# Kernel tuning notes

Hardware: AMD Instinct MI355X
Metric: run time of the kernel (lower is better)

## Reference

```python
import jax, jax.numpy as jnp
import numpy as np
from jax import lax


def _b_mask(out_c, in_c, kh, kw):
    # MaskedConv2d mask_type='B' for a 1xK kernel: zero strictly right-of-center taps
    m = np.ones((out_c, in_c, kh, kw), dtype=np.float32)
    m[:, :, kh // 2:, kw // 2 + 1:] = 0
    m[:, :, kh // 2 + 1:, :] = 0
    return jnp.asarray(m)


def _conv(x, w, b):
    # NCHW 'same' conv, stride 1
    y = lax.conv_general_dilated(x, w, (1, 1), 'SAME',
                                 dimension_numbers=('NCHW', 'OIHW', 'NCHW'))
    return y + b[None, :, None, None]


def setup_inputs() -> dict:
    key = jax.random.key(0)
    ks = jax.random.split(key, 7)
    B, C_in, H, W = 32, 3, 64, 64
    HC = 128
    return {
        'x': jax.random.normal(ks[0], (B, C_in, H, W), jnp.float32),
        'W_is': jax.random.normal(ks[1], (4 * HC, C_in, 1, 3), jnp.float32) * 0.1,
        'b_is': jax.random.normal(ks[2], (4 * HC,), jnp.float32) * 0.1,
        'W_ss': jax.random.normal(ks[3], (4 * HC, HC, 1, 3), jnp.float32) * 0.1,
        'b_ss': jax.random.normal(ks[4], (4 * HC,), jnp.float32) * 0.1,
        'h0': jax.random.normal(ks[5], (1, HC, 1, W), jnp.float32) * 0.05,
        'c0': jax.random.normal(ks[6], (1, HC, 1, W), jnp.float32) * 0.05,
    }


def reference(x, W_is, b_is, W_ss, b_ss, h0, c0):
    B, _, H, W = x.shape
    HC = h0.shape[1]
    W_is_m = W_is * _b_mask(*W_is.shape)
    W_ss_m = W_ss * _b_mask(*W_ss.shape)

    # input-to-state projection for all rows at once: [B, 4*HC, H, W]
    x_proj = _conv(x, W_is_m, b_is)
    x_rows = jnp.moveaxis(x_proj, 2, 0)[:, :, :, None, :]  # [H, B, 4HC, 1, W]

    h_init = jnp.broadcast_to(h0, (B, HC, 1, W))
    c_init = jnp.broadcast_to(c0, (B, HC, 1, W))

    def step(carry, row_x):
        h_prev, c_prev = carry
        gates = jax.nn.sigmoid(row_x + _conv(h_prev, W_ss_m, b_ss))
        o, f, i, g = jnp.split(gates, 4, axis=1)
        c = f * c_prev + i * g
        h = o * jnp.tanh(c)
        return (h, c), h

    _, hs = lax.scan(step, (h_init, c_init), x_rows)  # hs: [H, B, HC, 1, W]
    hidden = jnp.moveaxis(hs[:, :, :, 0, :], 0, 2)  # [B, HC, H, W]
    return hidden
```

## Files before the change

### kernel.cpp

```cpp
#include <hip/hip_runtime.h>
#include <hip/hip_bf16.h>

typedef unsigned short u16;
typedef unsigned int u32;
typedef unsigned long long u64;
typedef short bf16x8 __attribute__((ext_vector_type(8)));
typedef float f32x4  __attribute__((ext_vector_type(4)));


__device__ __forceinline__ u16 f2b(float f) {
    return __builtin_bit_cast(u16, __float2bfloat16(f));
}
__device__ __forceinline__ float sigm(float x) {
    return __builtin_amdgcn_rcpf(1.0f + __expf(-x));
}

#define LINE(kt, lane) (((kt) * 64 + (lane)) * 16)
#define BUFBYTES (8 * 64 * 16)
#define SPIN_CAP (1 << 16)

__global__ __launch_bounds__(512, 2) void rowlstm_mfma13(
    const float* __restrict__ x,   const float* __restrict__ Wis,
    const float* __restrict__ bis, const float* __restrict__ Wss,
    const float* __restrict__ bss, const float* __restrict__ h0,
    const float* __restrict__ c0,  float* __restrict__ out,
    char* halo)
{
    __shared__ __align__(16) char lds_buf[2 * BUFBYTES];
    __shared__ __align__(16) char lds_xpk[64 * 16 * 16];
    __shared__ u16  lds_x[3 * 64 * 17];
    __shared__ float lds_bias[512];

    const int tid  = threadIdx.x;
    const int s    = blockIdx.x;
    const int b    = blockIdx.y;
    const int wid  = tid >> 6;
    const int lane = tid & 63;
    const int q    = lane >> 4;
    const int n    = lane & 15;
    const int wbase = s * 16;

    char* hs_my = halo + ((size_t)(b * 4 + s) * 64) * 256;
    char* hs_up = halo + ((size_t)(b * 4 + (s > 0 ? s - 1 : 0)) * 64) * 256;

    for (int i = tid; i < 1024; i += 512)
        *(uint4*)(lds_buf + i * 16) = make_uint4(0, 0, 0, 0);
    __syncthreads();

    lds_bias[tid] = bis[tid] + bss[tid];

    for (int i = tid; i < 3264; i += 512) {
        int cch = i / 1088, rem = i % 1088;
        int r = rem / 17, wl1 = rem % 17;
        int gw = wbase + wl1 - 1;
        lds_x[i] = (gw < 0) ? (u16)0
                 : f2b(x[(((size_t)b * 3 + cch) * 64 + r) * 64 + gw]);
    }

    bf16x8 afr[4][9];
    {
        #pragma unroll
        for (int g = 0; g < 4; ++g) {
            int oc = g * 128 + wid * 16 + n;
            #pragma unroll
            for (int kt = 0; kt < 8; ++kt) {
                bf16x8 a;
                #pragma unroll
                for (int jj = 0; jj < 4; ++jj) {
                    int ic = kt * 16 + q * 4 + jj;
                    float2 wp = *(const float2*)&Wss[(size_t)(oc * 128 + ic) * 3];
                    a[jj]     = (short)f2b(wp.y);
                    a[4 + jj] = (short)f2b(wp.x);
                }
                afr[g][kt] = a;
            }
            bf16x8 ax = {0, 0, 0, 0, 0, 0, 0, 0};
            if (q == 0) {
                #pragma unroll
                for (int cch = 0; cch < 3; ++cch) {
                    float2 wp = *(const float2*)&Wis[(size_t)(oc * 3 + cch) * 3];
                    ax[cch]     = (short)f2b(wp.y);
                    ax[4 + cch] = (short)f2b(wp.x);
                }
            }
            afr[g][8] = ax;
        }
    }

    float cst[4];
    {
        u16 hw[4];
        #pragma unroll
        for (int reg = 0; reg < 4; ++reg) {
            int hc = wid * 16 + q * 4 + reg;
            int wg = wbase + n;
            cst[reg] = c0[hc * 64 + wg];
            hw[reg] = f2b(h0[hc * 64 + wg]);
        }
        u64 d01 = (u64)((u32)hw[0] | ((u32)hw[1] << 16))
                | ((u64)((u32)hw[2] | ((u32)hw[3] << 16)) << 32);
        *(u64*)(lds_buf + LINE(wid, lane)) = d01;
        int wl = n + 1;
        if (wl < 16)
            *(u64*)(lds_buf + LINE(wid, q * 16 + wl) + 8) = d01;
    }
    if (s > 0 && tid < 32) {
        int ic0 = tid * 4;
        u64 v = (u64)((u32)f2b(h0[(ic0 + 0) * 64 + wbase - 1]) | ((u32)f2b(h0[(ic0 + 1) * 64 + wbase - 1]) << 16))
              | ((u64)((u32)f2b(h0[(ic0 + 2) * 64 + wbase - 1]) | ((u32)f2b(h0[(ic0 + 3) * 64 + wbase - 1]) << 16)) << 32);
        *(u64*)(lds_buf + LINE(tid >> 2, (tid & 3) * 16) + 8) = v;
    }

    __syncthreads();

    #pragma unroll
    for (int t = 0; t < 2; ++t) {
        int slot = tid + t * 512;
        int r = slot >> 4, nn = slot & 15;
        u32 d0 = (u32)lds_x[0 * 1088 + r * 17 + nn + 1] | ((u32)lds_x[1 * 1088 + r * 17 + nn + 1] << 16);
        u32 d1 = (u32)lds_x[2 * 1088 + r * 17 + nn + 1];
        u32 d2 = (u32)lds_x[0 * 1088 + r * 17 + nn]     | ((u32)lds_x[1 * 1088 + r * 17 + nn] << 16);
        u32 d3 = (u32)lds_x[2 * 1088 + r * 17 + nn];
        *(uint4*)(lds_xpk + slot * 16) = make_uint4(d0, d1, d2, d3);
    }
    __syncthreads();

    f32x4 bias_r[4];
    #pragma unroll
    for (int g = 0; g < 4; ++g) {
        int oc = g * 128 + wid * 16 + q * 4;
        bias_r[g][0] = lds_bias[oc + 0];
        bias_r[g][1] = lds_bias[oc + 1];
        bias_r[g][2] = lds_bias[oc + 2];
        bias_r[g][3] = lds_bias[oc + 3];
    }

    u64 hv = 0, hn = 0;
    const bool is_cons = (s > 0) && (tid < 32);
    if (is_cons)
        hv = __hip_atomic_load((const u64*)(hs_up + (size_t)tid * 8),
                               __ATOMIC_RELAXED, __HIP_MEMORY_SCOPE_AGENT);

    for (int r = 0; r < 64; ++r) {
        char* rbuf = lds_buf + (r & 1) * BUFBYTES;
        char* wbuf = lds_buf + ((r & 1) ^ 1) * BUFBYTES;

        if (is_cons && r < 62)
            hn = __hip_atomic_load((const u64*)(hs_up + (size_t)(r + 1) * 256 + tid * 8),
                                   __ATOMIC_RELAXED, __HIP_MEMORY_SCOPE_AGENT);

        bf16x8 bv[9];
        #pragma unroll
        for (int kt = 0; kt < 8; ++kt)
            bv[kt] = *(const bf16x8*)(rbuf + LINE(kt, lane));
        bv[8] = *(const bf16x8*)(lds_xpk + r * 256 + n * 16);

        f32x4 acc[4];
        acc[0] = bias_r[0]; acc[1] = bias_r[1];
        acc[2] = bias_r[2]; acc[3] = bias_r[3];
        #pragma unroll
        for (int kt = 0; kt < 9; ++kt) {
            acc[0] = __builtin_amdgcn_mfma_f32_16x16x32_bf16(afr[0][kt], bv[kt], acc[0], 0, 0, 0);
            acc[1] = __builtin_amdgcn_mfma_f32_16x16x32_bf16(afr[1][kt], bv[kt], acc[1], 0, 0, 0);
            acc[2] = __builtin_amdgcn_mfma_f32_16x16x32_bf16(afr[2][kt], bv[kt], acc[2], 0, 0, 0);
            acc[3] = __builtin_amdgcn_mfma_f32_16x16x32_bf16(afr[3][kt], bv[kt], acc[3], 0, 0, 0);
        }

        float hval[4];
        #pragma unroll
        for (int reg = 0; reg < 4; ++reg) {
            float eo = __expf(-acc[0][reg]);
            float ef = __expf(-acc[1][reg]);
            float ei = __expf(-acc[2][reg]);
            float eg = __expf(-acc[3][reg]);
            float f_ = __builtin_amdgcn_rcpf(1.0f + ef);
            float t  = 1.0f + ei;
            float ig = __builtin_amdgcn_rcpf(__builtin_fmaf(eg, t, t));
            float cn = f_ * cst[reg] + ig;
            cst[reg] = cn;
            float o_ = __builtin_amdgcn_rcpf(1.0f + eo);
            float e2 = __expf(2.0f * cn);
            float th = 1.0f - 2.0f * __builtin_amdgcn_rcpf(e2 + 1.0f);
            hval[reg] = o_ * th;
        }

        u32 plo, phi;
        asm("v_cvt_pk_bf16_f32 %0, %1, %2" : "=v"(plo) : "v"(hval[0]), "v"(hval[1]));
        asm("v_cvt_pk_bf16_f32 %0, %1, %2" : "=v"(phi) : "v"(hval[2]), "v"(hval[3]));
        u64 d01 = (u64)plo | ((u64)phi << 32);

        *(u64*)(wbuf + LINE(wid, lane)) = d01;
        int wl = n + 1;
        if (wl < 16) {
            *(u64*)(wbuf + LINE(wid, q * 16 + wl) + 8) = d01;
        } else if (s < 3 && r < 63) {
            __hip_atomic_store((u64*)(hs_my + (size_t)r * 256 + (wid * 4 + q) * 8),
                               ~d01, __ATOMIC_RELAXED, __HIP_MEMORY_SCOPE_AGENT);
        }

        #pragma unroll
        for (int reg = 0; reg < 4; ++reg) {
            int hc = wid * 16 + q * 4 + reg;
            out[(((size_t)(b * 128 + hc)) * 64 + r) * 64 + wbase + n] = hval[reg];
        }

        if (is_cons && r < 63) {
            if (hv == 0) {
                int guard = 0;
                do {
                    __builtin_amdgcn_s_sleep(1);
                    hv = __hip_atomic_load((const u64*)(hs_up + (size_t)r * 256 + tid * 8),
                                           __ATOMIC_RELAXED, __HIP_MEMORY_SCOPE_AGENT);
                } while (hv == 0 && ++guard < SPIN_CAP);
            }
            *(u64*)(wbuf + LINE(tid >> 2, (tid & 3) * 16) + 8) = ~hv;
            hv = hn;
        }

        __builtin_amdgcn_sched_barrier(0);
        asm volatile("s_waitcnt lgkmcnt(0)\n\ts_barrier" ::: "memory");
        __builtin_amdgcn_sched_barrier(0);
    }
}

extern "C" void kernel_launch(void* const* d_in, const int* in_sizes, int n_in,
                              void* d_out, int out_size, void* d_ws, size_t ws_size,
                              hipStream_t stream)
{
    const float* x   = (const float*)d_in[0];
    const float* Wis = (const float*)d_in[1];
    const float* bis = (const float*)d_in[2];
    const float* Wss = (const float*)d_in[3];
    const float* bss = (const float*)d_in[4];
    const float* h0  = (const float*)d_in[5];
    const float* c0  = (const float*)d_in[6];
    float* out = (float*)d_out;

    hipMemsetAsync(d_ws, 0, (size_t)32 * 4 * 64 * 256, stream);
    rowlstm_mfma13<<<dim3(4, 32), 512, 0, stream>>>(
        x, Wis, bis, Wss, bss, h0, c0, out, (char*)d_ws);
}
```

Measured before the change: 203.2 us.

## Split gate computation across 16 waves with LDS flag handoff for i*g

Doubles the workgroup to 1024 threads. Back waves compute the input and cell gates (i, g) and pass i*g to front waves through LDS, signalled by a per-wave flag. Front waves compute o and f and carry out the cell/hidden update, the halo exchange and the output stores. This halves the MFMA chain and weight registers per wave to cut per-row latency on the serial recurrence, at the cost of intra-workgroup spin-waiting and an extra LDS round trip.

```diff
diff --git a/kernel.cpp b/kernel.cpp
--- a/kernel.cpp
+++ b/kernel.cpp
@@ -11,15 +11,12 @@
 __device__ __forceinline__ u16 f2b(float f) {
     return __builtin_bit_cast(u16, __float2bfloat16(f));
 }
-__device__ __forceinline__ float sigm(float x) {
-    return __builtin_amdgcn_rcpf(1.0f + __expf(-x));
-}
 
 #define LINE(kt, lane) (((kt) * 64 + (lane)) * 16)
 #define BUFBYTES (8 * 64 * 16)
 #define SPIN_CAP (1 << 16)
 
-__global__ __launch_bounds__(512, 2) void rowlstm_mfma13(
+__global__ __launch_bounds__(1024, 1) void rowlstm_mfma14(
     const float* __restrict__ x,   const float* __restrict__ Wis,
     const float* __restrict__ bis, const float* __restrict__ Wss,
     const float* __restrict__ bss, const float* __restrict__ h0,
@@ -28,13 +25,17 @@
 {
     __shared__ __align__(16) char lds_buf[2 * BUFBYTES];
     __shared__ __align__(16) char lds_xpk[64 * 16 * 16];
+    __shared__ __align__(16) char lds_igb[8 * 64 * 16];
     __shared__ u16  lds_x[3 * 64 * 17];
     __shared__ float lds_bias[512];
+    __shared__ u32  igf[8];
 
     const int tid  = threadIdx.x;
     const int s    = blockIdx.x;
     const int b    = blockIdx.y;
     const int wid  = tid >> 6;
+    const int p    = wid & 7;
+    const bool front = (wid < 8);
     const int lane = tid & 63;
     const int q    = lane >> 4;
     const int n    = lane & 15;
@@ -43,13 +44,14 @@
     char* hs_my = halo + ((size_t)(b * 4 + s) * 64) * 256;
     char* hs_up = halo + ((size_t)(b * 4 + (s > 0 ? s - 1 : 0)) * 64) * 256;
 
-    for (int i = tid; i < 1024; i += 512)
-        *(uint4*)(lds_buf + i * 16) = make_uint4(0, 0, 0, 0);
+    if (tid < 1024)
+        *(uint4*)(lds_buf + tid * 16) = make_uint4(0, 0, 0, 0);
+    if (tid < 8) igf[tid] = 0;
     __syncthreads();
 
-    lds_bias[tid] = bis[tid] + bss[tid];
-
-    for (int i = tid; i < 3264; i += 512) {
+    if (tid < 512) lds_bias[tid] = bis[tid] + bss[tid];
+
+    for (int i = tid; i < 3264; i += 1024) {
         int cch = i / 1088, rem = i % 1088;
         int r = rem / 17, wl1 = rem % 17;
         int gw = wbase + wl1 - 1;
@@ -57,11 +59,12 @@
                  : f2b(x[(((size_t)b * 3 + cch) * 64 + r) * 64 + gw]);
     }
 
-    bf16x8 afr[4][9];
+    const int gbase = front ? 0 : 2;
+    bf16x8 afr[2][9];
     {
         #pragma unroll
-        for (int g = 0; g < 4; ++g) {
-            int oc = g * 128 + wid * 16 + n;
+        for (int gg = 0; gg < 2; ++gg) {
+            int oc = (gbase + gg) * 128 + p * 16 + n;
             #pragma unroll
             for (int kt = 0; kt < 8; ++kt) {
                 bf16x8 a;
@@ -72,7 +75,7 @@
                     a[jj]     = (short)f2b(wp.y);
                     a[4 + jj] = (short)f2b(wp.x);
                 }
-                afr[g][kt] = a;
+                afr[gg][kt] = a;
             }
             bf16x8 ax = {0, 0, 0, 0, 0, 0, 0, 0};
             if (q == 0) {
@@ -83,26 +86,26 @@
                     ax[4 + cch] = (short)f2b(wp.x);
                 }
             }
-            afr[g][8] = ax;
-        }
-    }
-
-    float cst[4];
-    {
+            afr[gg][8] = ax;
+        }
+    }
+
+    float cst[4] = {0, 0, 0, 0};
+    if (front) {
         u16 hw[4];
         #pragma unroll
         for (int reg = 0; reg < 4; ++reg) {
-            int hc = wid * 16 + q * 4 + reg;
+            int hc = p * 16 + q * 4 + reg;
             int wg = wbase + n;
             cst[reg] = c0[hc * 64 + wg];
             hw[reg] = f2b(h0[hc * 64 + wg]);
         }
         u64 d01 = (u64)((u32)hw[0] | ((u32)hw[1] << 16))
                 | ((u64)((u32)hw[2] | ((u32)hw[3] << 16)) << 32);
-        *(u64*)(lds_buf + LINE(wid, lane)) = d01;
+        *(u64*)(lds_buf + LINE(p, lane)) = d01;
         int wl = n + 1;
         if (wl < 16)
-            *(u64*)(lds_buf + LINE(wid, q * 16 + wl) + 8) = d01;
+            *(u64*)(lds_buf + LINE(p, q * 16 + wl) + 8) = d01;
     }
     if (s > 0 && tid < 32) {
         int ic0 = tid * 4;
@@ -113,9 +116,8 @@
 
     __syncthreads();
 
-    #pragma unroll
-    for (int t = 0; t < 2; ++t) {
-        int slot = tid + t * 512;
+    {
+        int slot = tid;
         int r = slot >> 4, nn = slot & 15;
         u32 d0 = (u32)lds_x[0 * 1088 + r * 17 + nn + 1] | ((u32)lds_x[1 * 1088 + r * 17 + nn + 1] << 16);
         u32 d1 = (u32)lds_x[2 * 1088 + r * 17 + nn + 1];
@@ -125,14 +127,14 @@
     }
     __syncthreads();
 
-    f32x4 bias_r[4];
+    f32x4 bias_r[2];
     #pragma unroll
-    for (int g = 0; g < 4; ++g) {
-        int oc = g * 128 + wid * 16 + q * 4;
-        bias_r[g][0] = lds_bias[oc + 0];
-        bias_r[g][1] = lds_bias[oc + 1];
-        bias_r[g][2] = lds_bias[oc + 2];
-        bias_r[g][3] = lds_bias[oc + 3];
+    for (int gg = 0; gg < 2; ++gg) {
+        int oc = (gbase + gg) * 128 + p * 16 + q * 4;
+        bias_r[gg][0] = lds_bias[oc + 0];
+        bias_r[gg][1] = lds_bias[oc + 1];
+        bias_r[gg][2] = lds_bias[oc + 2];
+        bias_r[gg][3] = lds_bias[oc + 3];
     }
 
     u64 hv = 0, hn = 0;
@@ -155,66 +157,91 @@
             bv[kt] = *(const bf16x8*)(rbuf + LINE(kt, lane));
         bv[8] = *(const bf16x8*)(lds_xpk + r * 256 + n * 16);
 
-        f32x4 acc[4];
+        f32x4 acc[2];
         acc[0] = bias_r[0]; acc[1] = bias_r[1];
-        acc[2] = bias_r[2]; acc[3] = bias_r[3];
         #pragma unroll
         for (int kt = 0; kt < 9; ++kt) {
             acc[0] = __builtin_amdgcn_mfma_f32_16x16x32_bf16(afr[0][kt], bv[kt], acc[0], 0, 0, 0);
             acc[1] = __builtin_amdgcn_mfma_f32_16x16x32_bf16(afr[1][kt], bv[kt], acc[1], 0, 0, 0);
-            acc[2] = __builtin_amdgcn_mfma_f32_16x16x32_bf16(afr[2][kt], bv[kt], acc[2], 0, 0, 0);
-            acc[3] = __builtin_amdgcn_mfma_f32_16x16x32_bf16(afr[3][kt], bv[kt], acc[3], 0, 0, 0);
-        }
-
-        float hval[4];
-        #pragma unroll
-        for (int reg = 0; reg < 4; ++reg) {
-            float eo = __expf(-acc[0][reg]);
-            float ef = __expf(-acc[1][reg]);
-            float ei = __expf(-acc[2][reg]);
-            float eg = __expf(-acc[3][reg]);
-            float f_ = __builtin_amdgcn_rcpf(1.0f + ef);
-            float t  = 1.0f + ei;
-            float ig = __builtin_amdgcn_rcpf(__builtin_fmaf(eg, t, t));
-            float cn = f_ * cst[reg] + ig;
-            cst[reg] = cn;
-            float o_ = __builtin_amdgcn_rcpf(1.0f + eo);
-            float e2 = __expf(2.0f * cn);
-            float th = 1.0f - 2.0f * __builtin_amdgcn_rcpf(e2 + 1.0f);
-            hval[reg] = o_ * th;
-        }
-
-        u32 plo, phi;
-        asm("v_cvt_pk_bf16_f32 %0, %1, %2" : "=v"(plo) : "v"(hval[0]), "v"(hval[1]));
-        asm("v_cvt_pk_bf16_f32 %0, %1, %2" : "=v"(phi) : "v"(hval[2]), "v"(hval[3]));
-        u64 d01 = (u64)plo | ((u64)phi << 32);
-
-        *(u64*)(wbuf + LINE(wid, lane)) = d01;
-        int wl = n + 1;
-        if (wl < 16) {
-            *(u64*)(wbuf + LINE(wid, q * 16 + wl) + 8) = d01;
-        } else if (s < 3 && r < 63) {
-            __hip_atomic_store((u64*)(hs_my + (size_t)r * 256 + (wid * 4 + q) * 8),
-                               ~d01, __ATOMIC_RELAXED, __HIP_MEMORY_SCOPE_AGENT);
-        }
-
-        #pragma unroll
-        for (int reg = 0; reg < 4; ++reg) {
-            int hc = wid * 16 + q * 4 + reg;
-            out[(((size_t)(b * 128 + hc)) * 64 + r) * 64 + wbase + n] = hval[reg];
-        }
-
-        if (is_cons && r < 63) {
-            if (hv == 0) {
+        }
+
+        if (!front) {
+            f32x4 igv;
+            #pragma unroll
+            for (int reg = 0; reg < 4; ++reg) {
+                float ei = __expf(-acc[0][reg]);
+                float eg = __expf(-acc[1][reg]);
+                float t  = 1.0f + ei;
+                igv[reg] = __builtin_amdgcn_rcpf(__builtin_fmaf(eg, t, t));
+            }
+            *(f32x4*)(lds_igb + (p * 64 + lane) * 16) = igv;
+            __builtin_amdgcn_sched_barrier(0);
+            asm volatile("s_waitcnt lgkmcnt(0)" ::: "memory");
+            __builtin_amdgcn_sched_barrier(0);
+            if (lane == 0)
+                __hip_atomic_store(&igf[p], (u32)(r + 1), __ATOMIC_RELAXED,
+                                   __HIP_MEMORY_SCOPE_WORKGROUP);
+        } else {
+            u32 fv = __hip_atomic_load(&igf[p], __ATOMIC_RELAXED,
+                                       __HIP_MEMORY_SCOPE_WORKGROUP);
+            if (fv < (u32)(r + 1)) {
                 int guard = 0;
                 do {
                     __builtin_amdgcn_s_sleep(1);
-                    hv = __hip_atomic_load((const u64*)(hs_up + (size_t)r * 256 + tid * 8),
-                                           __ATOMIC_RELAXED, __HIP_MEMORY_SCOPE_AGENT);
-                } while (hv == 0 && ++guard < SPIN_CAP);
-            }
-            *(u64*)(wbuf + LINE(tid >> 2, (tid & 3) * 16) + 8) = ~hv;
-            hv = hn;
+                    fv = __hip_atomic_load(&igf[p], __ATOMIC_RELAXED,
+                                           __HIP_MEMORY_SCOPE_WORKGROUP);
+                } while (fv < (u32)(r + 1) && ++guard < SPIN_CAP);
+            }
+            int igo = (p * 64 + lane) * 16;
+            asm volatile("" : "+v"(igo) : "v"(fv));
+            f32x4 ig4 = *(const f32x4*)(lds_igb + igo);
+
+            float hval[4];
+            #pragma unroll
+            for (int reg = 0; reg < 4; ++reg) {
+                float eo = __expf(-acc[0][reg]);
+                float ef = __expf(-acc[1][reg]);
+                float f_ = __builtin_amdgcn_rcpf(1.0f + ef);
+                float cn = f_ * cst[reg] + ig4[reg];
+                cst[reg] = cn;
+                float o_ = __builtin_amdgcn_rcpf(1.0f + eo);
+                float e2 = __expf(2.0f * cn);
+                float th = 1.0f - 2.0f * __builtin_amdgcn_rcpf(e2 + 1.0f);
+                hval[reg] = o_ * th;
+            }
+
+            u32 plo, phi;
+            asm("v_cvt_pk_bf16_f32 %0, %1, %2" : "=v"(plo) : "v"(hval[0]), "v"(hval[1]));
+            asm("v_cvt_pk_bf16_f32 %0, %1, %2" : "=v"(phi) : "v"(hval[2]), "v"(hval[3]));
+            u64 d01 = (u64)plo | ((u64)phi << 32);
+
+            *(u64*)(wbuf + LINE(p, lane)) = d01;
+            int wl = n + 1;
+            if (wl < 16) {
+                *(u64*)(wbuf + LINE(p, q * 16 + wl) + 8) = d01;
+            } else if (s < 3 && r < 63) {
+                __hip_atomic_store((u64*)(hs_my + (size_t)r * 256 + (p * 4 + q) * 8),
+                                   ~d01, __ATOMIC_RELAXED, __HIP_MEMORY_SCOPE_AGENT);
+            }
+
+            #pragma unroll
+            for (int reg = 0; reg < 4; ++reg) {
+                int hc = p * 16 + q * 4 + reg;
+                out[(((size_t)(b * 128 + hc)) * 64 + r) * 64 + wbase + n] = hval[reg];
+            }
+
+            if (is_cons && r < 63) {
+                if (hv == 0) {
+                    int guard = 0;
+                    do {
+                        __builtin_amdgcn_s_sleep(1);
+                        hv = __hip_atomic_load((const u64*)(hs_up + (size_t)r * 256 + tid * 8),
+                                               __ATOMIC_RELAXED, __HIP_MEMORY_SCOPE_AGENT);
+                    } while (hv == 0 && ++guard < SPIN_CAP);
+                }
+                *(u64*)(wbuf + LINE(tid >> 2, (tid & 3) * 16) + 8) = ~hv;
+                hv = hn;
+            }
         }
 
         __builtin_amdgcn_sched_barrier(0);
@@ -237,6 +264,6 @@
     float* out = (float*)d_out;
 
     hipMemsetAsync(d_ws, 0, (size_t)32 * 4 * 64 * 256, stream);
-    rowlstm_mfma13<<<dim3(4, 32), 512, 0, stream>>>(
+    rowlstm_mfma14<<<dim3(4, 32), 1024, 0, stream>>>(
         x, Wis, bis, Wss, bss, h0, c0, out, (char*)d_ws);
 }
```

Measured after the change: 225.3 us. +10.9%, slower.
